# Optimization experiments

Measured on AMD Instinct MI355X. Metric: run time of the kernel, lower is better.

## Reference

```python
import jax, jax.numpy as jnp
import numpy as np

DIM = 64
N_ENTITY = 1000000
N_RELATION = 32
L = 2
B = 4096
K = 64


def setup_inputs() -> dict:
    key = jax.random.key(0)
    ks = jax.random.split(key, 24)
    s = 0.05
    d = DIM
    inp = {
        "items": jax.random.randint(ks[0], (B,), 0, N_ENTITY),
        "heads": jax.random.randint(ks[1], (L, B, K), 0, N_ENTITY),
        "relations": jax.random.randint(ks[2], (L, B, K), 0, N_RELATION),
        "tails": jax.random.randint(ks[3], (L, B, K), 0, N_ENTITY),
        # learned parameters
        "embedding": jax.random.normal(ks[4], (N_ENTITY, d), jnp.float32) * s,
        "transformer": jax.random.normal(ks[5], (N_RELATION, d), jnp.float32) * s,
        "attn_w": jax.random.normal(ks[6], (1, 3 * d), jnp.float32) * s,
        "attn_b": jax.random.normal(ks[7], (1,), jnp.float32) * s,
        "W_ih": jax.random.normal(ks[8], (d, d), jnp.float32) * s,
        "W_hh": jax.random.normal(ks[9], (d, d), jnp.float32) * s,
        "b_ih": jax.random.normal(ks[10], (d,), jnp.float32) * s,
        "b_hh": jax.random.normal(ks[11], (d,), jnp.float32) * s,
        "l1_w": jax.random.normal(ks[12], (d, 2 * d), jnp.float32) * s,
        "l1_b": jax.random.normal(ks[13], (d,), jnp.float32) * s,
        "l2_w": jax.random.normal(ks[14], (d, d), jnp.float32) * s,
        "l2_b": jax.random.normal(ks[15], (d,), jnp.float32) * s,
        "l3_w": jax.random.normal(ks[16], (d, d), jnp.float32) * s,
        "l3_b": jax.random.normal(ks[17], (d,), jnp.float32) * s,
        "lin_w": jax.random.normal(ks[18], (1, 2 * d), jnp.float32) * s,
        "lin_b": jax.random.normal(ks[19], (1,), jnp.float32) * s,
    }
    return inp


def _ncfg_forward(embedding, transformer, attn_w, attn_b, W_ih, W_hh, b_ih, b_hh,
                  l1_w, l1_b, l2_w, l2_b, l3_w, l3_b, lin_w, lin_b,
                  items, heads, relations, tails):
    o_sum = jnp.zeros((B, DIM), embedding.dtype)
    for l in range(L):
        h = embedding[heads[l]]          # [B, K, d]
        r = transformer[relations[l]]    # [B, K, d]
        tl = embedding[tails[l]]         # [B, K, d]
        hRt = jnp.concatenate([h, r, tl], axis=-1)                  # [B, K, 3d]
        pi = jax.nn.sigmoid(hRt @ attn_w.T + attn_b)                # [B, K, 1]
        pi = jax.nn.softmax(pi, axis=1)                             # softmax over neighbors
        # 2-step tanh RNN over seq (head, tail), h0 = 0
        h1 = jnp.tanh(h @ W_ih.T + b_ih + b_hh)                     # [B, K, d]
        h2 = jnp.tanh(tl @ W_ih.T + b_ih + h1 @ W_hh.T + b_hh)      # [B, K, d]
        o_sum = o_sum + (pi * h2).sum(axis=1)                       # [B, d]
    user_emb = o_sum
    item_emb = embedding[items]                                     # [B, d]
    # NCF head (dropout in eval mode = identity)
    ui = jnp.concatenate([user_emb, item_emb], axis=-1)             # [B, 2d]
    y = jax.nn.relu(ui @ l1_w.T + l1_b)
    y = jax.nn.relu(y @ l2_w.T + l2_b)
    y1 = jax.nn.sigmoid(y @ l3_w.T + l3_b)
    y2 = user_emb * item_emb
    out = jax.nn.sigmoid(jnp.concatenate([y1, y2], axis=-1) @ lin_w.T + lin_b)
    return out[:, 0]  # squeeze -> [B]


def reference(items, heads, relations, tails, embedding, transformer, attn_w, attn_b,
              W_ih, W_hh, b_ih, b_hh, l1_w, l1_b, l2_w, l2_b, l3_w, l3_b, lin_w, lin_b):
    return _ncfg_forward(embedding, transformer, attn_w, attn_b, W_ih, W_hh, b_ih, b_hh,
                         l1_w, l1_b, l2_w, l2_b, l3_w, l3_b, lin_w, lin_b,
                         items, heads, relations, tails)
```

## Files before the change

kernel.cpp:

```cpp
#include <hip/hip_runtime.h>
#include <hip/hip_bf16.h>
#include <cstdint>
#include <cstddef>

#define B_SZ 4096

typedef __attribute__((ext_vector_type(4))) float f32x4;
typedef __attribute__((ext_vector_type(8))) short sv8;
typedef __attribute__((ext_vector_type(8))) __bf16 bfv8;

__device__ __align__(16) short g_wf[2][8][64][8];
__device__ __align__(16) short g_af[2][2][64][8];
__device__ float g_bsum[64];
__device__ float g_reldot[32];

static __device__ __forceinline__ short f2bf(float x) {
  union { float f; unsigned u; } v; v.f = x;
  unsigned r = v.u + 0x7fffu + ((v.u >> 16) & 1u);
  return (short)(r >> 16);
}
static __device__ __forceinline__ short f2bfc(float x) {
  return (short)__builtin_bit_cast(unsigned short, __float2bfloat16(x));
}

static __device__ __forceinline__ f32x4 MFMA(sv8 a, sv8 b, f32x4 c) {
  return __builtin_amdgcn_mfma_f32_16x16x32_bf16(
      __builtin_bit_cast(bfv8, a), __builtin_bit_cast(bfv8, b), c, 0, 0, 0);
}

static __device__ __forceinline__ float fast_sigmoid(float x) {
  return __builtin_amdgcn_rcpf(1.f + __expf(-x));
}
static __device__ __forceinline__ float fast_tanh(float x) {
  const float e = __expf(2.f * x);
  return 1.f - 2.f * __builtin_amdgcn_rcpf(e + 1.f);
}
static __device__ __forceinline__ sv8 pack8(f32x4 a, f32x4 b) {
  sv8 f;
  f[0] = f2bfc(a.x); f[1] = f2bfc(a.y); f[2] = f2bfc(a.z); f[3] = f2bfc(a.w);
  f[4] = f2bfc(b.x); f[5] = f2bfc(b.y); f[6] = f2bfc(b.z); f[7] = f2bfc(b.w);
  return f;
}

__global__ __launch_bounds__(256) void ncfg_prep(
    const float* __restrict__ W_ih, const float* __restrict__ W_hh,
    const float* __restrict__ b_ih, const float* __restrict__ b_hh,
    const float* __restrict__ trf, const float* __restrict__ attn_w) {
  const int t = threadIdx.x;
  for (int q = t; q < 1024; q += 256) {
    const int m = q >> 9, f = (q >> 6) & 7, ln = q & 63;
    const int nt = f >> 1, kh = f & 1, fr = ln & 15, fg = ln >> 4;
    const float* W = m ? W_hh : W_ih;
    const float* src = W + (nt * 16 + fr) * 64 + kh * 32 + fg * 8;
    short* dst = &g_wf[m][f][ln][0];
    #pragma unroll
    for (int j = 0; j < 8; ++j) dst[j] = f2bf(src[j]);
  }
  {
    const int a = t >> 7, kh = (t >> 6) & 1, ln = t & 63;
    const int n = ln & 15, kf = ln >> 4;
    short* dst = &g_af[a][kh][ln][0];
    #pragma unroll
    for (int j = 0; j < 8; ++j)
      dst[j] = (n == 0) ? f2bf(attn_w[a * 128 + kh * 32 + kf * 8 + j]) : (short)0;
  }
  if (t < 64) g_bsum[t] = b_ih[t] + b_hh[t];
  if (t < 32) {
    float s = 0.f;
    #pragma unroll 8
    for (int c = 0; c < 64; ++c) s += trf[t * 64 + c] * attn_w[64 + c];
    g_reldot[t] = s;
  }
}

__global__ __launch_bounds__(256, 4) void ncfg_neigh(
    const int* __restrict__ heads, const int* __restrict__ rels,
    const int* __restrict__ tails, const float* __restrict__ emb,
    const float* __restrict__ attn_b, float* __restrict__ opart) {
  const int t = threadIdx.x;
  const int lane = t & 63;
  const int w = t >> 6;
  const int fr = lane & 15;
  const int fg = lane >> 4;
  const int c0 = fg * 8;

  __shared__ __align__(16) short wlds[2][8][64][8];
  __shared__ __align__(16) short alds[2][2][64][8];
  __shared__ float rlds[32];
  __shared__ __align__(16) short h1s[4][16 * 72];
  __shared__ float ow[4][64];
  __shared__ float sew[4];

  const size_t ibase = (size_t)blockIdx.x * 64;

  const int hi = heads[ibase + (w << 4) + fr];
  const int ti = tails[ibase + (w << 4) + fr];
  const int ri = rels[ibase + (w << 4) + fr];

  {
    const f32x4* s1 = (const f32x4*)&g_wf[0][0][0][0];
    f32x4* d1 = (f32x4*)&wlds[0][0][0][0];
    #pragma unroll
    for (int i = 0; i < 4; ++i) d1[t + i * 256] = s1[t + i * 256];
    const f32x4* s2 = (const f32x4*)&g_af[0][0][0][0];
    ((f32x4*)&alds[0][0][0][0])[t] = s2[t];
    if (t < 8) ((f32x4*)rlds)[t] = ((const f32x4*)g_reldot)[t];
  }

  float bsum[4];
  #pragma unroll
  for (int nt = 0; nt < 4; ++nt) bsum[nt] = g_bsum[nt * 16 + fr];
  const float ab0 = attn_b[0];

  const float* hr = emb + (size_t)hi * 64;
  const float* tr = emb + (size_t)ti * 64;
  const f32x4 h0 = *(const f32x4*)(hr + c0);
  const f32x4 h1 = *(const f32x4*)(hr + c0 + 4);
  const f32x4 h2 = *(const f32x4*)(hr + 32 + c0);
  const f32x4 h3 = *(const f32x4*)(hr + 32 + c0 + 4);
  const f32x4 t0 = *(const f32x4*)(tr + c0);
  const f32x4 t1 = *(const f32x4*)(tr + c0 + 4);
  const f32x4 t2 = *(const f32x4*)(tr + 32 + c0);
  const f32x4 t3 = *(const f32x4*)(tr + 32 + c0 + 4);

  __syncthreads();

  const sv8 ha0 = pack8(h0, h1), ha1 = pack8(h2, h3);
  const sv8 ta0 = pack8(t0, t1), ta1 = pack8(t2, t3);

  const f32x4 zz = {0.f, 0.f, 0.f, 0.f};

  f32x4 accl = zz;
  accl = MFMA(ha0, *(const sv8*)&alds[0][0][lane][0], accl);
  accl = MFMA(ha1, *(const sv8*)&alds[0][1][lane][0], accl);
  accl = MFMA(ta0, *(const sv8*)&alds[1][0][lane][0], accl);
  accl = MFMA(ta1, *(const sv8*)&alds[1][1][lane][0], accl);

  f32x4 ev;
  #pragma unroll
  for (int r = 0; r < 4; ++r) {
    const float lg = __shfl(accl[r], fg << 4);
    const int rr = __shfl(ri, (fg << 2) + r);
    ev[r] = __expf(fast_sigmoid(lg + rlds[rr] + ab0));
  }
  float se = ev.x + ev.y + ev.z + ev.w;

  f32x4 acc[4] = {zz, zz, zz, zz};
  #pragma unroll
  for (int nt = 0; nt < 4; ++nt)
    acc[nt] = MFMA(ha0, *(const sv8*)&wlds[0][nt * 2][lane][0], acc[nt]);
  #pragma unroll
  for (int nt = 0; nt < 4; ++nt)
    acc[nt] = MFMA(ha1, *(const sv8*)&wlds[0][nt * 2 + 1][lane][0], acc[nt]);
  #pragma unroll
  for (int nt = 0; nt < 4; ++nt)
    #pragma unroll
    for (int r = 0; r < 4; ++r)
      h1s[w][((fg << 2) + r) * 72 + nt * 16 + fr] =
          f2bfc(fast_tanh(acc[nt][r] + bsum[nt]));

  f32x4 acc2[4] = {zz, zz, zz, zz};
  #pragma unroll
  for (int nt = 0; nt < 4; ++nt)
    acc2[nt] = MFMA(ta0, *(const sv8*)&wlds[0][nt * 2][lane][0], acc2[nt]);
  #pragma unroll
  for (int nt = 0; nt < 4; ++nt)
    acc2[nt] = MFMA(ta1, *(const sv8*)&wlds[0][nt * 2 + 1][lane][0], acc2[nt]);
  const sv8 a1 = *(const sv8*)&h1s[w][fr * 72 + c0];
  const sv8 a2 = *(const sv8*)&h1s[w][fr * 72 + 32 + c0];
  #pragma unroll
  for (int nt = 0; nt < 4; ++nt)
    acc2[nt] = MFMA(a1, *(const sv8*)&wlds[1][nt * 2][lane][0], acc2[nt]);
  #pragma unroll
  for (int nt = 0; nt < 4; ++nt)
    acc2[nt] = MFMA(a2, *(const sv8*)&wlds[1][nt * 2 + 1][lane][0], acc2[nt]);

  #pragma unroll
  for (int nt = 0; nt < 4; ++nt) {
    float s = ev.x * fast_tanh(acc2[nt][0] + bsum[nt]) +
              ev.y * fast_tanh(acc2[nt][1] + bsum[nt]) +
              ev.z * fast_tanh(acc2[nt][2] + bsum[nt]) +
              ev.w * fast_tanh(acc2[nt][3] + bsum[nt]);
    s += __shfl_xor(s, 16);
    s += __shfl_xor(s, 32);
    if (fg == 0) ow[w][nt * 16 + fr] = s;
  }
  se += __shfl_xor(se, 16);
  se += __shfl_xor(se, 32);
  if (lane == 0) sew[w] = se;

  __syncthreads();

  if (w == 0) {
    const float o = ow[0][lane] + ow[1][lane] + ow[2][lane] + ow[3][lane];
    const float st = sew[0] + sew[1] + sew[2] + sew[3];
    opart[ibase + lane] = o * __builtin_amdgcn_rcpf(st);
  }
}

__global__ __launch_bounds__(256) void ncfg_head(
    const float* __restrict__ opart, const float* __restrict__ emb,
    const int* __restrict__ items, const float* __restrict__ l1_w,
    const float* __restrict__ l1_b, const float* __restrict__ l2_w,
    const float* __restrict__ l2_b, const float* __restrict__ l3_w,
    const float* __restrict__ l3_b, const float* __restrict__ lin_w,
    const float* __restrict__ lin_b, float* __restrict__ out) {
  const int wv = threadIdx.x >> 6;
  const int i = threadIdx.x & 63;
  const int b = blockIdx.x * 4 + wv;

  __shared__ float ui[4][128];
  __shared__ float yy[4][64];

  const float ue = opart[(size_t)b * 64 + i] +
                   opart[((size_t)B_SZ + b) * 64 + i];
  const float ie = emb[(size_t)items[b] * 64 + i];
  ui[wv][i] = ue;
  ui[wv][64 + i] = ie;
  __syncthreads();

  float acc = l1_b[i];
  {
    const float* wr = l1_w + i * 128;
    #pragma unroll
    for (int j = 0; j < 128; j += 4) {
      const f32x4 wvv = *(const f32x4*)(wr + j);
      const f32x4 uv = *(const f32x4*)&ui[wv][j];
      acc += wvv.x * uv.x + wvv.y * uv.y + wvv.z * uv.z + wvv.w * uv.w;
    }
  }
  float y = fmaxf(acc, 0.f);
  yy[wv][i] = y;
  __syncthreads();

  acc = l2_b[i];
  {
    const float* wr = l2_w + i * 64;
    #pragma unroll
    for (int j = 0; j < 64; j += 4) {
      const f32x4 wvv = *(const f32x4*)(wr + j);
      const f32x4 uv = *(const f32x4*)&yy[wv][j];
      acc += wvv.x * uv.x + wvv.y * uv.y + wvv.z * uv.z + wvv.w * uv.w;
    }
  }
  y = fmaxf(acc, 0.f);
  __syncthreads();
  yy[wv][i] = y;
  __syncthreads();

  acc = l3_b[i];
  {
    const float* wr = l3_w + i * 64;
    #pragma unroll
    for (int j = 0; j < 64; j += 4) {
      const f32x4 wvv = *(const f32x4*)(wr + j);
      const f32x4 uv = *(const f32x4*)&yy[wv][j];
      acc += wvv.x * uv.x + wvv.y * uv.y + wvv.z * uv.z + wvv.w * uv.w;
    }
  }
  const float y1 = fast_sigmoid(acc);
  const float y2 = ue * ie;

  float part = y1 * lin_w[i] + y2 * lin_w[64 + i];
  #pragma unroll
  for (int m = 1; m < 64; m <<= 1) part += __shfl_xor(part, m);
  if (i == 0) out[b] = fast_sigmoid(part + lin_b[0]);
}

extern "C" void kernel_launch(void* const* d_in, const int* in_sizes, int n_in,
                              void* d_out, int out_size, void* d_ws,
                              size_t ws_size, hipStream_t stream) {
  (void)in_sizes; (void)n_in; (void)out_size; (void)ws_size;
  const int* items = (const int*)d_in[0];
  const int* heads = (const int*)d_in[1];
  const int* rels = (const int*)d_in[2];
  const int* tails = (const int*)d_in[3];
  const float* emb = (const float*)d_in[4];
  const float* trf = (const float*)d_in[5];
  const float* attn_w = (const float*)d_in[6];
  const float* attn_b = (const float*)d_in[7];
  const float* W_ih = (const float*)d_in[8];
  const float* W_hh = (const float*)d_in[9];
  const float* b_ih = (const float*)d_in[10];
  const float* b_hh = (const float*)d_in[11];
  const float* l1_w = (const float*)d_in[12];
  const float* l1_b = (const float*)d_in[13];
  const float* l2_w = (const float*)d_in[14];
  const float* l2_b = (const float*)d_in[15];
  const float* l3_w = (const float*)d_in[16];
  const float* l3_b = (const float*)d_in[17];
  const float* lin_w = (const float*)d_in[18];
  const float* lin_b = (const float*)d_in[19];
  float* out = (float*)d_out;
  float* opart = (float*)d_ws;

  ncfg_prep<<<dim3(1), dim3(256), 0, stream>>>(W_ih, W_hh, b_ih, b_hh, trf,
                                               attn_w);
  ncfg_neigh<<<dim3(2 * B_SZ), dim3(256), 0, stream>>>(
      heads, rels, tails, emb, attn_b, opart);
  ncfg_head<<<dim3(B_SZ / 4), dim3(256), 0, stream>>>(
      opart, emb, items, l1_w, l1_b, l2_w, l2_b, l3_w, l3_b, lin_w, lin_b,
      out);
}
```

Before: 85.18 us.

## Compute attention logits with fp32 dot products and shrink LDS for occupancy

Replaces the four zero-padded MFMAs that computed attention logits with per-lane fp32 dot products against attn_w staged in LDS, followed by cross-lane shuffle reductions. The padded bf16 attention-weight fragments and their prep code are removed. The per-wave output and softmax-sum buffers now reuse the h1s scratch region, and the occupancy hint in launch bounds goes from 4 to 6 blocks per CU. The intent is to cut MFMA work and LDS footprint so more blocks fit per CU, at the cost of more VALU and shuffle instructions and tighter register limits.

```diff
diff --git a/kernel.cpp b/kernel.cpp
--- a/kernel.cpp
+++ b/kernel.cpp
@@ -10,7 +10,6 @@
 typedef __attribute__((ext_vector_type(8))) __bf16 bfv8;
 
 __device__ __align__(16) short g_wf[2][8][64][8];
-__device__ __align__(16) short g_af[2][2][64][8];
 __device__ float g_bsum[64];
 __device__ float g_reldot[32];
 
@@ -34,6 +33,9 @@
 static __device__ __forceinline__ float fast_tanh(float x) {
   const float e = __expf(2.f * x);
   return 1.f - 2.f * __builtin_amdgcn_rcpf(e + 1.f);
+}
+static __device__ __forceinline__ float dot4(f32x4 a, f32x4 b) {
+  return a.x * b.x + a.y * b.y + a.z * b.z + a.w * b.w;
 }
 static __device__ __forceinline__ sv8 pack8(f32x4 a, f32x4 b) {
   sv8 f;
@@ -56,14 +58,6 @@
     #pragma unroll
     for (int j = 0; j < 8; ++j) dst[j] = f2bf(src[j]);
   }
-  {
-    const int a = t >> 7, kh = (t >> 6) & 1, ln = t & 63;
-    const int n = ln & 15, kf = ln >> 4;
-    short* dst = &g_af[a][kh][ln][0];
-    #pragma unroll
-    for (int j = 0; j < 8; ++j)
-      dst[j] = (n == 0) ? f2bf(attn_w[a * 128 + kh * 32 + kf * 8 + j]) : (short)0;
-  }
   if (t < 64) g_bsum[t] = b_ih[t] + b_hh[t];
   if (t < 32) {
     float s = 0.f;
@@ -73,10 +67,11 @@
   }
 }
 
-__global__ __launch_bounds__(256, 4) void ncfg_neigh(
+__global__ __launch_bounds__(256, 6) void ncfg_neigh(
     const int* __restrict__ heads, const int* __restrict__ rels,
     const int* __restrict__ tails, const float* __restrict__ emb,
-    const float* __restrict__ attn_b, float* __restrict__ opart) {
+    const float* __restrict__ attn_w, const float* __restrict__ attn_b,
+    float* __restrict__ opart) {
   const int t = threadIdx.x;
   const int lane = t & 63;
   const int w = t >> 6;
@@ -85,11 +80,9 @@
   const int c0 = fg * 8;
 
   __shared__ __align__(16) short wlds[2][8][64][8];
-  __shared__ __align__(16) short alds[2][2][64][8];
+  __shared__ __align__(16) float awlds[192];
   __shared__ float rlds[32];
   __shared__ __align__(16) short h1s[4][16 * 72];
-  __shared__ float ow[4][64];
-  __shared__ float sew[4];
 
   const size_t ibase = (size_t)blockIdx.x * 64;
 
@@ -102,8 +95,7 @@
     f32x4* d1 = (f32x4*)&wlds[0][0][0][0];
     #pragma unroll
     for (int i = 0; i < 4; ++i) d1[t + i * 256] = s1[t + i * 256];
-    const f32x4* s2 = (const f32x4*)&g_af[0][0][0][0];
-    ((f32x4*)&alds[0][0][0][0])[t] = s2[t];
+    if (t < 48) ((f32x4*)awlds)[t] = ((const f32x4*)attn_w)[t];
     if (t < 8) ((f32x4*)rlds)[t] = ((const f32x4*)g_reldot)[t];
   }
 
@@ -125,25 +117,28 @@
 
   __syncthreads();
 
+  float ap = dot4(h0, *(const f32x4*)&awlds[c0]) +
+             dot4(h1, *(const f32x4*)&awlds[c0 + 4]) +
+             dot4(h2, *(const f32x4*)&awlds[32 + c0]) +
+             dot4(h3, *(const f32x4*)&awlds[32 + c0 + 4]) +
+             dot4(t0, *(const f32x4*)&awlds[128 + c0]) +
+             dot4(t1, *(const f32x4*)&awlds[128 + c0 + 4]) +
+             dot4(t2, *(const f32x4*)&awlds[160 + c0]) +
+             dot4(t3, *(const f32x4*)&awlds[160 + c0 + 4]);
+  ap += __shfl_xor(ap, 16);
+  ap += __shfl_xor(ap, 32);
+
+  const float e_own = __expf(fast_sigmoid(ap + rlds[ri] + ab0));
+  float se = e_own;
+  se += __shfl_xor(se, 1);
+  se += __shfl_xor(se, 2);
+  se += __shfl_xor(se, 4);
+  se += __shfl_xor(se, 8);
+
   const sv8 ha0 = pack8(h0, h1), ha1 = pack8(h2, h3);
   const sv8 ta0 = pack8(t0, t1), ta1 = pack8(t2, t3);
 
   const f32x4 zz = {0.f, 0.f, 0.f, 0.f};
-
-  f32x4 accl = zz;
-  accl = MFMA(ha0, *(const sv8*)&alds[0][0][lane][0], accl);
-  accl = MFMA(ha1, *(const sv8*)&alds[0][1][lane][0], accl);
-  accl = MFMA(ta0, *(const sv8*)&alds[1][0][lane][0], accl);
-  accl = MFMA(ta1, *(const sv8*)&alds[1][1][lane][0], accl);
-
-  f32x4 ev;
-  #pragma unroll
-  for (int r = 0; r < 4; ++r) {
-    const float lg = __shfl(accl[r], fg << 4);
-    const int rr = __shfl(ri, (fg << 2) + r);
-    ev[r] = __expf(fast_sigmoid(lg + rlds[rr] + ab0));
-  }
-  float se = ev.x + ev.y + ev.z + ev.w;
 
   f32x4 acc[4] = {zz, zz, zz, zz};
   #pragma unroll
@@ -159,6 +154,10 @@
       h1s[w][((fg << 2) + r) * 72 + nt * 16 + fr] =
           f2bfc(fast_tanh(acc[nt][r] + bsum[nt]));
 
+  f32x4 ev;
+  #pragma unroll
+  for (int r = 0; r < 4; ++r) ev[r] = __shfl(e_own, (fg << 2) + r);
+
   f32x4 acc2[4] = {zz, zz, zz, zz};
   #pragma unroll
   for (int nt = 0; nt < 4; ++nt)
@@ -175,6 +174,7 @@
   for (int nt = 0; nt < 4; ++nt)
     acc2[nt] = MFMA(a2, *(const sv8*)&wlds[1][nt * 2 + 1][lane][0], acc2[nt]);
 
+  float* owp = (float*)&h1s[w][0];
   #pragma unroll
   for (int nt = 0; nt < 4; ++nt) {
     float s = ev.x * fast_tanh(acc2[nt][0] + bsum[nt]) +
@@ -183,17 +183,20 @@
               ev.w * fast_tanh(acc2[nt][3] + bsum[nt]);
     s += __shfl_xor(s, 16);
     s += __shfl_xor(s, 32);
-    if (fg == 0) ow[w][nt * 16 + fr] = s;
-  }
-  se += __shfl_xor(se, 16);
-  se += __shfl_xor(se, 32);
-  if (lane == 0) sew[w] = se;
+    if (fg == 0) owp[nt * 16 + fr] = s;
+  }
+  if (lane == 0) owp[64] = se;
 
   __syncthreads();
 
   if (w == 0) {
-    const float o = ow[0][lane] + ow[1][lane] + ow[2][lane] + ow[3][lane];
-    const float st = sew[0] + sew[1] + sew[2] + sew[3];
+    float o = 0.f, st = 0.f;
+    #pragma unroll
+    for (int q = 0; q < 4; ++q) {
+      const float* p = (const float*)&h1s[q][0];
+      o += p[lane];
+      st += p[64];
+    }
     opart[ibase + lane] = o * __builtin_amdgcn_rcpf(st);
   }
 }
@@ -297,7 +300,7 @@
   ncfg_prep<<<dim3(1), dim3(256), 0, stream>>>(W_ih, W_hh, b_ih, b_hh, trf,
                                                attn_w);
   ncfg_neigh<<<dim3(2 * B_SZ), dim3(256), 0, stream>>>(
-      heads, rels, tails, emb, attn_b, opart);
+      heads, rels, tails, emb, attn_w, attn_b, opart);
   ncfg_head<<<dim3(B_SZ / 4), dim3(256), 0, stream>>>(
       opart, emb, items, l1_w, l1_b, l2_w, l2_b, l3_w, l3_b, lin_w, lin_b,
       out);
```

Result: no change. 84.07 us (-1.3%).
